# Optimization experiments

Hardware: AMD Instinct MI355X
Metric: run time of the kernel (lower is better)

## Reference

```python
import jax, jax.numpy as jnp
import numpy as np

N, E = 50000, 800000
F_IN, EDGE_DIM, H, C = 128, 64, 8, 32
NEG_SLOPE = 0.2


def setup_inputs() -> dict:
    key = jax.random.key(0)
    ks = jax.random.split(key, 9)
    return {
        "x": jax.random.normal(ks[0], (N, F_IN), dtype=jnp.float32),
        "edge_index": jax.random.randint(ks[1], (2, E), 0, N, dtype=jnp.int32),
        "edge_attr": jax.random.normal(ks[2], (E, EDGE_DIM), dtype=jnp.float32),
        "W": jax.random.normal(ks[3], (F_IN, H * C), dtype=jnp.float32) * 0.05,
        "att_src": jax.random.normal(ks[4], (H, C), dtype=jnp.float32) * 0.05,
        "att_dst": jax.random.normal(ks[5], (H, C), dtype=jnp.float32) * 0.05,
        "W_edge": jax.random.normal(ks[6], (EDGE_DIM, H * C), dtype=jnp.float32) * 0.05,
        "att_edge": jax.random.normal(ks[7], (H, C), dtype=jnp.float32) * 0.05,
        "bias": jax.random.normal(ks[8], (H * C,), dtype=jnp.float32) * 0.05,
    }


def reference(x, edge_index, edge_attr, W, att_src, att_dst, W_edge, att_edge, bias):
    src, dst = edge_index[0], edge_index[1]  # messages flow src -> dst
    # Pre-activation ReLU from Graph_intra.forward
    xr = jax.nn.relu(x)
    # Linear projection, per-head view: [N, H, C]
    xs = (xr @ W).reshape(N, H, C)
    # Per-node attention logits: [N, H]
    a_src = jnp.einsum("nhc,hc->nh", xs, att_src)
    a_dst = jnp.einsum("nhc,hc->nh", xs, att_dst)
    # Edge-feature attention contribution: [E, H]
    e_proj = (edge_attr @ W_edge).reshape(E, H, C)
    a_edge = jnp.einsum("ehc,hc->eh", e_proj, att_edge)
    # Per-edge logits + LeakyReLU
    alpha = jax.nn.leaky_relu(a_src[src] + a_dst[dst] + a_edge, NEG_SLOPE)  # [E, H]
    # Segment softmax over destination neighborhoods
    seg_max = jax.ops.segment_max(alpha, dst, num_segments=N)
    seg_max = jnp.where(jnp.isfinite(seg_max), seg_max, 0.0)
    alpha = jnp.exp(alpha - seg_max[dst])
    seg_sum = jax.ops.segment_sum(alpha, dst, num_segments=N)
    alpha = alpha / (seg_sum[dst] + 1e-16)
    # Weighted message aggregation: scatter-add alpha_e * x_src[e]
    msgs = alpha[:, :, None] * xs[src]  # [E, H, C]
    out = jax.ops.segment_sum(msgs, dst, num_segments=N)  # [N, H, C]
    return out.reshape(N, H * C) + bias
```

## Files before the change

### kernel.cpp

```cpp
#include <hip/hip_runtime.h>

#define N_NODES 50000
#define E_EDGES 800000
#define F_IN    128
#define EDGE_DIM 64
#define HC      256
#define NEG_SLOPE 0.2f

typedef __attribute__((ext_vector_type(8))) short short8;
typedef __attribute__((ext_vector_type(4))) float f32x4;

__device__ __forceinline__ unsigned short f2bf(float f) {
    unsigned u = __builtin_bit_cast(unsigned, f);
    u += 0x7fffu + ((u >> 16) & 1u);
    return (unsigned short)(u >> 16);
}
__device__ __forceinline__ float bf2f(unsigned short b) {
    return __builtin_bit_cast(float, (unsigned)b << 16);
}

__global__ __launch_bounds__(256) void k_pre(const float* __restrict__ W,
        const float* __restrict__ att_src, const float* __restrict__ att_dst,
        const float* __restrict__ W_edge, const float* __restrict__ att_edge,
        unsigned short* __restrict__ W_T, unsigned short* __restrict__ WaT,
        float* __restrict__ We_fold, int* __restrict__ counts, int* __restrict__ gcur) {
    int idx = blockIdx.x * 256 + threadIdx.x;
    if (idx < N_NODES) counts[idx] = 0;
    if (idx == 0) *gcur = 0;
    if (idx < 32768) {
        int n = idx >> 7, k = idx & 127;
        W_T[n * 128 + k] = f2bf(W[k * 256 + n]);
    }
    if (idx < 2048) {
        int col = idx & 15, k = idx >> 4;
        const float* att = (col < 8) ? att_src : att_dst;
        int h = col & 7;
        float s = 0.f;
        #pragma unroll
        for (int c = 0; c < 32; ++c)
            s = fmaf(W[k * 256 + h * 32 + c], att[h * 32 + c], s);
        WaT[col * 128 + k] = f2bf(s);
    }
    if (idx < 512) {
        int d = idx >> 3, h = idx & 7;
        float s = 0.f;
        #pragma unroll
        for (int c = 0; c < 32; ++c)
            s = fmaf(W_edge[d * 256 + h * 32 + c], att_edge[h * 32 + c], s);
        We_fold[d * 8 + h] = s;
    }
}

#define NT_TILES 782
#define K1_GRID 512
#define HIST_BLOCKS 782
__global__ __launch_bounds__(256, 2) void k1h(const float* __restrict__ x,
        const unsigned short* __restrict__ W_T, const unsigned short* __restrict__ WaT,
        const int4* __restrict__ dst4, int* __restrict__ counts,
        unsigned short* __restrict__ xs, float* __restrict__ a_src, float* __restrict__ a_dst) {
    __shared__ unsigned short sB[256 * 128];
    __shared__ unsigned short sA[64 * 128];
    int t = threadIdx.x;

    if (blockIdx.x < HIST_BLOCKS) {
        int i = blockIdx.x * 256 + t;
        if (i < E_EDGES / 4) {
            int4 d = dst4[i];
            atomicAdd(&counts[d.x], 1);
            atomicAdd(&counts[d.y], 1);
            atomicAdd(&counts[d.z], 1);
            atomicAdd(&counts[d.w], 1);
        }
        return;
    }
    int bid = blockIdx.x - HIST_BLOCKS;

    for (int G = t; G < 4096; G += 256) {
        int n = G >> 4, gi = G & 15;
        *(int4*)&sB[(n * 16 + (gi ^ (n & 7))) * 8] = *(const int4*)&W_T[n * 128 + gi * 8];
    }
    int lane = t & 63, w = t >> 6, mr = lane & 15, g = lane >> 4;
    short8 wa[4];
    #pragma unroll
    for (int ks = 0; ks < 4; ++ks)
        wa[ks] = *(const short8*)&WaT[mr * 128 + ks * 32 + g * 8];

    bool first = true;
    for (int rt = bid; rt < NT_TILES; rt += K1_GRID) {
        if (!first) __syncthreads();
        first = false;
        for (int G = t; G < 1024; G += 256) {
            int r = G >> 4, gi = G & 15;
            int node = rt * 64 + r;
            unsigned short pk[8];
            if (node < N_NODES) {
                const float* xp = &x[(long)node * 128 + gi * 8];
                #pragma unroll
                for (int jj = 0; jj < 8; ++jj) pk[jj] = f2bf(fmaxf(xp[jj], 0.f));
            } else {
                #pragma unroll
                for (int jj = 0; jj < 8; ++jj) pk[jj] = 0;
            }
            *(int4*)&sA[(r * 16 + (gi ^ (r & 7))) * 8] = *(int4*)pk;
        }
        __syncthreads();

        f32x4 acc[17];
        #pragma unroll
        for (int i = 0; i < 17; ++i) acc[i] = (f32x4){0.f, 0.f, 0.f, 0.f};

        int r16 = w * 16 + mr;
        #pragma unroll
        for (int ks = 0; ks < 4; ++ks) {
            int pos = (ks * 4 + g) ^ (mr & 7);
            short8 a = *(const short8*)&sA[(r16 * 16 + pos) * 8];
            #pragma unroll
            for (int nt = 0; nt < 16; ++nt) {
                short8 b = *(const short8*)&sB[((nt * 16 + mr) * 16 + pos) * 8];
                acc[nt] = __builtin_amdgcn_mfma_f32_16x16x32_bf16(a, b, acc[nt], 0, 0, 0);
            }
            acc[16] = __builtin_amdgcn_mfma_f32_16x16x32_bf16(a, wa[ks], acc[16], 0, 0, 0);
        }

        #pragma unroll
        for (int r = 0; r < 4; ++r) {
            int node = rt * 64 + w * 16 + g * 4 + r;
            if (node < N_NODES) {
                #pragma unroll
                for (int nt = 0; nt < 16; ++nt)
                    xs[(long)node * 256 + nt * 16 + mr] = f2bf(acc[nt][r]);
                if (mr < 8) a_src[node * 8 + mr]       = acc[16][r];
                else        a_dst[node * 8 + (mr - 8)] = acc[16][r];
            }
        }
    }
}

__global__ __launch_bounds__(256) void k4_alloc(const int* __restrict__ counts,
                                                int* __restrict__ starts,
                                                int* __restrict__ cursor,
                                                int* __restrict__ gcur) {
    int n = blockIdx.x * 256 + threadIdx.x;
    int c = (n < N_NODES) ? counts[n] : 0;
    int incl = c;
    #pragma unroll
    for (int off = 1; off < 64; off <<= 1) {
        int u = __shfl_up(incl, off);
        if ((threadIdx.x & 63) >= off) incl += u;
    }
    int total = __shfl(incl, 63);
    int wavebase = 0;
    if ((threadIdx.x & 63) == 63) wavebase = atomicAdd(gcur, total);
    wavebase = __shfl(wavebase, 63);
    if (n < N_NODES) {
        int st = wavebase + incl - c;
        starts[n] = st;
        cursor[n] = st;
    }
}

#define K25_TILES 8
__global__ __launch_bounds__(256) void k25_fused(const float4* __restrict__ edge_attr4,
        const float* __restrict__ We_fold,
        const int* __restrict__ src, const int* __restrict__ dst,
        const float* __restrict__ a_src, const float* __restrict__ a_dst,
        int* __restrict__ cursor,
        _Float16* __restrict__ w_perm, int* __restrict__ src_perm) {
    __shared__ __align__(16) float se[32 * 68];
    __shared__ __align__(16) float sfT[8 * 68];
    __shared__ int s_src[32], s_dst[32], s_pos[32];
    int t = threadIdx.x;
    for (int i = t; i < 512; i += 256)
        sfT[(i & 7) * 68 + (i >> 3)] = We_fold[i];

    int e = t >> 3, h = t & 7;
    #pragma unroll 1
    for (int it = 0; it < K25_TILES; ++it) {
        long ebase = (long)blockIdx.x * (32 * K25_TILES) + it * 32;
        __syncthreads();
        for (int i = t; i < 512; i += 256) {
            float4 v = edge_attr4[ebase * 16 + i];
            *(float4*)&se[(i >> 4) * 68 + (i & 15) * 4] = v;
        }
        if (t < 32) {
            int ee = ebase + t;
            int d = dst[ee];
            s_src[t] = src[ee];
            s_dst[t] = d;
            s_pos[t] = atomicAdd(&cursor[d], 1);
        }
        __syncthreads();

        const float4* sa = (const float4*)&se[e * 68];
        const float4* sb = (const float4*)&sfT[h * 68];
        float s = 0.f;
        #pragma unroll
        for (int i = 0; i < 16; ++i) {
            float4 a = sa[i], b = sb[i];
            s = fmaf(a.x, b.x, s);
            s = fmaf(a.y, b.y, s);
            s = fmaf(a.z, b.z, s);
            s = fmaf(a.w, b.w, s);
        }
        int sn = s_src[e], dn = s_dst[e];
        float v = s + a_src[sn * 8 + h] + a_dst[dn * 8 + h];
        v = (v > 0.f) ? v : NEG_SLOPE * v;
        float w = __expf(v);
        int pos = s_pos[e];
        __builtin_nontemporal_store((_Float16)w, &w_perm[(size_t)pos * 8 + h]);
        if (h == 0) __builtin_nontemporal_store(sn, &src_perm[pos]);
    }
}

__global__ __launch_bounds__(256) void k6_wave(
    const int* __restrict__ starts, const int* __restrict__ counts,
    const _Float16* __restrict__ w_perm, const int* __restrict__ src_perm,
    const unsigned short* __restrict__ xs, const float* __restrict__ bias,
    float* __restrict__ out) {
    int lane = threadIdx.x & 63;
    int n = blockIdx.x * 4 + (threadIdx.x >> 6);
    if (n >= N_NODES) return;
    int start = starts[n], cnt = counts[n];
    int j = lane >> 3;
    int hq = lane >> 3;

    float acc0 = 0.f, acc1 = 0.f, acc2 = 0.f, acc3 = 0.f;
    float psum = 0.f;
    for (int base = 0; base < cnt; base += 8) {
        int nk = cnt - base; if (nk > 8) nk = 8;
        float wv = (float)__builtin_nontemporal_load(&w_perm[(size_t)(start + base) * 8 + lane]);
        if (j >= nk) wv = 0.f;
        psum += wv;
        int sv = __builtin_nontemporal_load(&src_perm[start + base + (lane & 7)]);
        #pragma unroll
        for (int jj = 0; jj < 8; ++jj) {
            int s = __shfl(sv, jj);
            s = (jj < nk) ? s : 0;
            float w = __shfl(wv, jj * 8 + hq);
            ushort4 xv = *(const ushort4*)&xs[(size_t)s * 256 + lane * 4];
            acc0 = fmaf(w, bf2f(xv.x), acc0);
            acc1 = fmaf(w, bf2f(xv.y), acc1);
            acc2 = fmaf(w, bf2f(xv.z), acc2);
            acc3 = fmaf(w, bf2f(xv.w), acc3);
        }
    }
    psum += __shfl_xor(psum, 8);
    psum += __shfl_xor(psum, 16);
    psum += __shfl_xor(psum, 32);
    float denom = __shfl(psum, hq);
    float rinv = 1.0f / (denom + 1e-16f);
    float4 bv = *(const float4*)&bias[lane * 4];
    f32x4 o;
    o[0] = acc0 * rinv + bv.x;
    o[1] = acc1 * rinv + bv.y;
    o[2] = acc2 * rinv + bv.z;
    o[3] = acc3 * rinv + bv.w;
    __builtin_nontemporal_store(o, (f32x4*)&out[(size_t)n * 256 + lane * 4]);
}

extern "C" void kernel_launch(void* const* d_in, const int* in_sizes, int n_in,
                              void* d_out, int out_size, void* d_ws, size_t ws_size,
                              hipStream_t stream) {
    const float* x         = (const float*)d_in[0];
    const int*   ei        = (const int*)d_in[1];
    const float* edge_attr = (const float*)d_in[2];
    const float* W         = (const float*)d_in[3];
    const float* att_src   = (const float*)d_in[4];
    const float* att_dst   = (const float*)d_in[5];
    const float* W_edge    = (const float*)d_in[6];
    const float* att_edge  = (const float*)d_in[7];
    const float* bias      = (const float*)d_in[8];
    float* out = (float*)d_out;

    const int* e_src = ei;
    const int* e_dst = ei + E_EDGES;

    char* p = (char*)d_ws;
    unsigned short* xs = (unsigned short*)p; p += (size_t)N_NODES * HC * 2;
    float* a_src   = (float*)p; p += (size_t)N_NODES * 8 * 4;
    float* a_dst   = (float*)p; p += (size_t)N_NODES * 8 * 4;
    _Float16* w_perm = (_Float16*)p; p += (size_t)E_EDGES * 8 * 2 + 256;
    int* src_perm  = (int*)p;   p += (size_t)E_EDGES * 4 + 256;
    unsigned short* W_T  = (unsigned short*)p; p += 32768 * 2;
    unsigned short* WaT  = (unsigned short*)p; p += 2048 * 2;
    float* We_fold = (float*)p; p += 512 * 4;
    int* counts    = (int*)p;   p += 200192;
    int* starts    = (int*)p;   p += 200192;
    int* cursor    = (int*)p;   p += 200192;
    int* gcur      = (int*)p;   p += 256;

    hipLaunchKernelGGL(k_pre, dim3(196), dim3(256), 0, stream,
                       W, att_src, att_dst, W_edge, att_edge, W_T, WaT, We_fold, counts, gcur);
    hipLaunchKernelGGL(k1h, dim3(HIST_BLOCKS + K1_GRID), dim3(256), 0, stream,
                       x, W_T, WaT, (const int4*)e_dst, counts, xs, a_src, a_dst);
    hipLaunchKernelGGL(k4_alloc, dim3(196), dim3(256), 0, stream,
                       counts, starts, cursor, gcur);
    hipLaunchKernelGGL(k25_fused, dim3(E_EDGES / (32 * K25_TILES)), dim3(256), 0, stream,
                       (const float4*)edge_attr, We_fold, e_src, e_dst,
                       a_src, a_dst, cursor, w_perm, src_perm);
    hipLaunchKernelGGL(k6_wave, dim3(N_NODES / 4), dim3(256), 0, stream,
                       starts, counts, w_perm, src_perm, xs, bias, out);
}
```

Baseline: 222.8 us.

## Reuse histogram atomic results as edge slots, drop cursor atomics in scatter

The histogram pass now stores the return value of each atomicAdd as that edge's slot within its destination bucket. The scatter kernel then computes each edge's position as starts[dst]+slot instead of doing a second atomic on a cursor array. The scatter kernel also goes from 8 tiles per block to one tile per block, and the nontemporal load/store hints are dropped. This trades 800K contended atomics for an extra 3.2MB slot array that is written once and read once.

```diff
diff --git a/kernel.cpp b/kernel.cpp
--- a/kernel.cpp
+++ b/kernel.cpp
@@ -56,7 +56,7 @@
 #define HIST_BLOCKS 782
 __global__ __launch_bounds__(256, 2) void k1h(const float* __restrict__ x,
         const unsigned short* __restrict__ W_T, const unsigned short* __restrict__ WaT,
-        const int4* __restrict__ dst4, int* __restrict__ counts,
+        const int4* __restrict__ dst4, int* __restrict__ counts, int4* __restrict__ slot4,
         unsigned short* __restrict__ xs, float* __restrict__ a_src, float* __restrict__ a_dst) {
     __shared__ unsigned short sB[256 * 128];
     __shared__ unsigned short sA[64 * 128];
@@ -66,10 +66,12 @@
         int i = blockIdx.x * 256 + t;
         if (i < E_EDGES / 4) {
             int4 d = dst4[i];
-            atomicAdd(&counts[d.x], 1);
-            atomicAdd(&counts[d.y], 1);
-            atomicAdd(&counts[d.z], 1);
-            atomicAdd(&counts[d.w], 1);
+            int4 sl;
+            sl.x = atomicAdd(&counts[d.x], 1);
+            sl.y = atomicAdd(&counts[d.y], 1);
+            sl.z = atomicAdd(&counts[d.z], 1);
+            sl.w = atomicAdd(&counts[d.w], 1);
+            slot4[i] = sl;
         }
         return;
     }
@@ -138,7 +140,6 @@
 
 __global__ __launch_bounds__(256) void k4_alloc(const int* __restrict__ counts,
                                                 int* __restrict__ starts,
-                                                int* __restrict__ cursor,
                                                 int* __restrict__ gcur) {
     int n = blockIdx.x * 256 + threadIdx.x;
     int c = (n < N_NODES) ? counts[n] : 0;
@@ -152,64 +153,53 @@
     int wavebase = 0;
     if ((threadIdx.x & 63) == 63) wavebase = atomicAdd(gcur, total);
     wavebase = __shfl(wavebase, 63);
-    if (n < N_NODES) {
-        int st = wavebase + incl - c;
-        starts[n] = st;
-        cursor[n] = st;
-    }
-}
-
-#define K25_TILES 8
+    if (n < N_NODES) starts[n] = wavebase + incl - c;
+}
+
 __global__ __launch_bounds__(256) void k25_fused(const float4* __restrict__ edge_attr4,
         const float* __restrict__ We_fold,
         const int* __restrict__ src, const int* __restrict__ dst,
+        const int* __restrict__ slot, const int* __restrict__ starts,
         const float* __restrict__ a_src, const float* __restrict__ a_dst,
-        int* __restrict__ cursor,
         _Float16* __restrict__ w_perm, int* __restrict__ src_perm) {
     __shared__ __align__(16) float se[32 * 68];
     __shared__ __align__(16) float sfT[8 * 68];
-    __shared__ int s_src[32], s_dst[32], s_pos[32];
+    __shared__ int s_src[32], s_dstn[32], s_pos[32];
     int t = threadIdx.x;
+    long ebase = (long)blockIdx.x * 32;
     for (int i = t; i < 512; i += 256)
         sfT[(i & 7) * 68 + (i >> 3)] = We_fold[i];
-
+    for (int i = t; i < 512; i += 256) {
+        float4 v = edge_attr4[ebase * 16 + i];
+        *(float4*)&se[(i >> 4) * 68 + (i & 15) * 4] = v;
+    }
+    if (t < 32) {
+        int ee = ebase + t;
+        int dn = dst[ee];
+        s_dstn[t] = dn;
+        s_src[t] = src[ee];
+        s_pos[t] = starts[dn] + slot[ee];
+    }
+    __syncthreads();
     int e = t >> 3, h = t & 7;
-    #pragma unroll 1
-    for (int it = 0; it < K25_TILES; ++it) {
-        long ebase = (long)blockIdx.x * (32 * K25_TILES) + it * 32;
-        __syncthreads();
-        for (int i = t; i < 512; i += 256) {
-            float4 v = edge_attr4[ebase * 16 + i];
-            *(float4*)&se[(i >> 4) * 68 + (i & 15) * 4] = v;
-        }
-        if (t < 32) {
-            int ee = ebase + t;
-            int d = dst[ee];
-            s_src[t] = src[ee];
-            s_dst[t] = d;
-            s_pos[t] = atomicAdd(&cursor[d], 1);
-        }
-        __syncthreads();
-
-        const float4* sa = (const float4*)&se[e * 68];
-        const float4* sb = (const float4*)&sfT[h * 68];
-        float s = 0.f;
-        #pragma unroll
-        for (int i = 0; i < 16; ++i) {
-            float4 a = sa[i], b = sb[i];
-            s = fmaf(a.x, b.x, s);
-            s = fmaf(a.y, b.y, s);
-            s = fmaf(a.z, b.z, s);
-            s = fmaf(a.w, b.w, s);
-        }
-        int sn = s_src[e], dn = s_dst[e];
-        float v = s + a_src[sn * 8 + h] + a_dst[dn * 8 + h];
-        v = (v > 0.f) ? v : NEG_SLOPE * v;
-        float w = __expf(v);
-        int pos = s_pos[e];
-        __builtin_nontemporal_store((_Float16)w, &w_perm[(size_t)pos * 8 + h]);
-        if (h == 0) __builtin_nontemporal_store(sn, &src_perm[pos]);
-    }
+    const float4* sa = (const float4*)&se[e * 68];
+    const float4* sb = (const float4*)&sfT[h * 68];
+    float s = 0.f;
+    #pragma unroll
+    for (int i = 0; i < 16; ++i) {
+        float4 a = sa[i], b = sb[i];
+        s = fmaf(a.x, b.x, s);
+        s = fmaf(a.y, b.y, s);
+        s = fmaf(a.z, b.z, s);
+        s = fmaf(a.w, b.w, s);
+    }
+    int sn = s_src[e], dn = s_dstn[e];
+    float v = s + a_src[sn * 8 + h] + a_dst[dn * 8 + h];
+    v = (v > 0.f) ? v : NEG_SLOPE * v;
+    float w = __expf(v);
+    int pos = s_pos[e];
+    w_perm[(size_t)pos * 8 + h] = (_Float16)w;
+    if (h == 0) src_perm[pos] = sn;
 }
 
 __global__ __launch_bounds__(256) void k6_wave(
@@ -228,10 +218,10 @@
     float psum = 0.f;
     for (int base = 0; base < cnt; base += 8) {
         int nk = cnt - base; if (nk > 8) nk = 8;
-        float wv = (float)__builtin_nontemporal_load(&w_perm[(size_t)(start + base) * 8 + lane]);
+        float wv = (float)w_perm[(size_t)(start + base) * 8 + lane];
         if (j >= nk) wv = 0.f;
         psum += wv;
-        int sv = __builtin_nontemporal_load(&src_perm[start + base + (lane & 7)]);
+        int sv = src_perm[start + base + (lane & 7)];
         #pragma unroll
         for (int jj = 0; jj < 8; ++jj) {
             int s = __shfl(sv, jj);
@@ -281,23 +271,23 @@
     float* a_dst   = (float*)p; p += (size_t)N_NODES * 8 * 4;
     _Float16* w_perm = (_Float16*)p; p += (size_t)E_EDGES * 8 * 2 + 256;
     int* src_perm  = (int*)p;   p += (size_t)E_EDGES * 4 + 256;
+    int* slot      = (int*)p;   p += (size_t)E_EDGES * 4 + 256;
     unsigned short* W_T  = (unsigned short*)p; p += 32768 * 2;
     unsigned short* WaT  = (unsigned short*)p; p += 2048 * 2;
     float* We_fold = (float*)p; p += 512 * 4;
     int* counts    = (int*)p;   p += 200192;
     int* starts    = (int*)p;   p += 200192;
-    int* cursor    = (int*)p;   p += 200192;
     int* gcur      = (int*)p;   p += 256;
 
     hipLaunchKernelGGL(k_pre, dim3(196), dim3(256), 0, stream,
                        W, att_src, att_dst, W_edge, att_edge, W_T, WaT, We_fold, counts, gcur);
     hipLaunchKernelGGL(k1h, dim3(HIST_BLOCKS + K1_GRID), dim3(256), 0, stream,
-                       x, W_T, WaT, (const int4*)e_dst, counts, xs, a_src, a_dst);
+                       x, W_T, WaT, (const int4*)e_dst, counts, (int4*)slot, xs, a_src, a_dst);
     hipLaunchKernelGGL(k4_alloc, dim3(196), dim3(256), 0, stream,
-                       counts, starts, cursor, gcur);
-    hipLaunchKernelGGL(k25_fused, dim3(E_EDGES / (32 * K25_TILES)), dim3(256), 0, stream,
-                       (const float4*)edge_attr, We_fold, e_src, e_dst,
-                       a_src, a_dst, cursor, w_perm, src_perm);
+                       counts, starts, gcur);
+    hipLaunchKernelGGL(k25_fused, dim3(E_EDGES / 32), dim3(256), 0, stream,
+                       (const float4*)edge_attr, We_fold, e_src, e_dst, slot, starts,
+                       a_src, a_dst, w_perm, src_perm);
     hipLaunchKernelGGL(k6_wave, dim3(N_NODES / 4), dim3(256), 0, stream,
                        starts, counts, w_perm, src_perm, xs, bias, out);
 }
```

After: 208.5 us. 6.4% less time.
